# Kernel optimization log

Hardware: AMD Instinct MI355X
Metric: run time of the kernel (lower is better)

## Reference

```python
import jax, jax.numpy as jnp
import numpy as np

EPS = 0.0  # init eps

def setup_inputs() -> dict:
    key = jax.random.key(0)
    k1, k2, k3 = jax.random.split(key, 3)
    n_nodes = 100000
    n_edges = 6400000
    edge_weight = jax.random.uniform(k1, (n_edges,), dtype=jnp.float32)  # non-negative, required by norm='both'
    src = jax.random.randint(k2, (n_edges,), 0, n_nodes, dtype=jnp.int32)
    dst = jax.random.randint(k3, (n_edges,), 0, n_nodes, dtype=jnp.int32)
    return {"edge_weight": edge_weight, "src": src, "dst": dst, "num_nodes": n_nodes}

def reference(edge_weight, src, dst, num_nodes):
    # norm='both': out-degree (weighted) per source node via reversed graph,
    # in-degree (weighted) per destination node; both as segment sums over edges.
    out_deg = jax.ops.segment_sum(edge_weight, src, num_segments=num_nodes) + EPS
    in_deg = jax.ops.segment_sum(edge_weight, dst, num_segments=num_nodes) + EPS
    src_norm = out_deg ** -0.5  # [N]
    dst_norm = in_deg ** -0.5   # [N]
    # gather per-edge norms and multiply with edge weight
    return src_norm[src] * dst_norm[dst] * edge_weight
```

## Files before the change

kernel.cpp:

```cpp
#include <hip/hip_runtime.h>
#include <hip/hip_fp16.h>


#define N_NODES 100000
#define TWO_N   (2 * N_NODES)
#define THREADS 1024
#define GBLK    1024
#define KMAX    7
#define SCALE_F   512.0f
#define INV_SCALE 0.001953125f

__global__ __launch_bounds__(THREADS)
void hist_kernel(const float4* __restrict__ w4,
                 const int4* __restrict__ src4,
                 const int4* __restrict__ dst4,
                 const float* __restrict__ w,
                 const int* __restrict__ src,
                 const int* __restrict__ dst,
                 unsigned* __restrict__ parts,
                 int n4, int n_edges, int P, int C, int bins, int chunk4,
                 int swz)
{
    extern __shared__ unsigned lds[];
    int j, c;
    if (swz) {
        const int x = blockIdx.x & 7;
        const int r = blockIdx.x >> 3;
        j = r % P;
        c = x + 8 * (r / P);
    } else {
        j = blockIdx.x / C;
        c = blockIdx.x - j * C;
    }
    const int lo = j * bins;

    for (int k = threadIdx.x; k < bins; k += THREADS) lds[k] = 0;
    __syncthreads();

    const int beg = c * chunk4;
    const int end = min(n4, beg + chunk4);

#define QUAD(wv, sv, dv)                                                      \
    do {                                                                      \
        unsigned v0 = (unsigned)((wv).x * SCALE_F + 0.5f);                    \
        unsigned v1 = (unsigned)((wv).y * SCALE_F + 0.5f);                    \
        unsigned v2 = (unsigned)((wv).z * SCALE_F + 0.5f);                    \
        unsigned v3 = (unsigned)((wv).w * SCALE_F + 0.5f);                    \
        int a0 = (sv).x - lo, a1 = (sv).y - lo, a2 = (sv).z - lo, a3 = (sv).w - lo; \
        int b0 = (dv).x - lo, b1 = (dv).y - lo, b2 = (dv).z - lo, b3 = (dv).w - lo; \
        if ((unsigned)a0 < (unsigned)bins) atomicAdd(&lds[a0], v0);           \
        if ((unsigned)a1 < (unsigned)bins) atomicAdd(&lds[a1], v1);           \
        if ((unsigned)a2 < (unsigned)bins) atomicAdd(&lds[a2], v2);           \
        if ((unsigned)a3 < (unsigned)bins) atomicAdd(&lds[a3], v3);           \
        if ((unsigned)b0 < (unsigned)bins) atomicAdd(&lds[b0], v0 << 16);     \
        if ((unsigned)b1 < (unsigned)bins) atomicAdd(&lds[b1], v1 << 16);     \
        if ((unsigned)b2 < (unsigned)bins) atomicAdd(&lds[b2], v2 << 16);     \
        if ((unsigned)b3 < (unsigned)bins) atomicAdd(&lds[b3], v3 << 16);     \
    } while (0)

    int i = beg + (int)threadIdx.x;
    for (; i + 3 * THREADS < end; i += 4 * THREADS) {
        float4 wa = w4[i];
        float4 wb = w4[i + THREADS];
        float4 wc = w4[i + 2 * THREADS];
        float4 wd = w4[i + 3 * THREADS];
        int4 sa = src4[i];
        int4 sb = src4[i + THREADS];
        int4 sc = src4[i + 2 * THREADS];
        int4 sd = src4[i + 3 * THREADS];
        int4 da = dst4[i];
        int4 db = dst4[i + THREADS];
        int4 dc = dst4[i + 2 * THREADS];
        int4 dd = dst4[i + 3 * THREADS];
        QUAD(wa, sa, da);
        QUAD(wb, sb, db);
        QUAD(wc, sc, dc);
        QUAD(wd, sd, dd);
    }
    for (; i < end; i += THREADS) {
        float4 wa = w4[i];
        int4 sa = src4[i];
        int4 da = dst4[i];
        QUAD(wa, sa, da);
    }
#undef QUAD

    if (c == C - 1 && threadIdx.x == 0) {
        for (int e = n4 * 4; e < n_edges; ++e) {
            unsigned v = (unsigned)(w[e] * SCALE_F + 0.5f);
            int a = src[e] - lo;
            int b = dst[e] - lo;
            if ((unsigned)a < (unsigned)bins) atomicAdd(&lds[a], v);
            if ((unsigned)b < (unsigned)bins) atomicAdd(&lds[b], v << 16);
        }
    }

    __syncthreads();
    unsigned* op = parts + ((size_t)j * C + c) * bins;
    for (int k = threadIdx.x; k < bins; k += THREADS)
        __builtin_nontemporal_store(lds[k], op + k);
}

__global__ void reduce_rsqrt_kernel(const unsigned* __restrict__ parts,
                                    __half* __restrict__ normh,
                                    int P, int C, int bins)
{
    int i = blockIdx.x * blockDim.x + threadIdx.x;
    if (i >= N_NODES) return;
    int p = i / bins;
    int b = i - p * bins;
    const unsigned* base = parts + ((size_t)p * C) * bins + b;
    unsigned lo0 = 0, hi0 = 0, lo1 = 0, hi1 = 0, lo2 = 0, hi2 = 0, lo3 = 0, hi3 = 0;
    int c = 0;
    for (; c + 3 < C; c += 4) {
        unsigned v0 = base[(size_t)(c + 0) * bins];
        unsigned v1 = base[(size_t)(c + 1) * bins];
        unsigned v2 = base[(size_t)(c + 2) * bins];
        unsigned v3 = base[(size_t)(c + 3) * bins];
        lo0 += v0 & 0xFFFFu; hi0 += v0 >> 16;
        lo1 += v1 & 0xFFFFu; hi1 += v1 >> 16;
        lo2 += v2 & 0xFFFFu; hi2 += v2 >> 16;
        lo3 += v3 & 0xFFFFu; hi3 += v3 >> 16;
    }
    for (; c < C; ++c) {
        unsigned v = base[(size_t)c * bins];
        lo0 += v & 0xFFFFu; hi0 += v >> 16;
    }
    unsigned lo_s = lo0 + lo1 + lo2 + lo3;
    unsigned hi_s = hi0 + hi1 + hi2 + hi3;
    normh[i]           = __float2half(1.0f / sqrtf((float)lo_s * INV_SCALE));
    normh[N_NODES + i] = __float2half(1.0f / sqrtf((float)hi_s * INV_SCALE));
}

__global__ void degree_atomic_kernel(const float* __restrict__ w,
                                     const int* __restrict__ src,
                                     const int* __restrict__ dst,
                                     float* __restrict__ deg,
                                     int n_edges)
{
    int i = blockIdx.x * blockDim.x + threadIdx.x;
    int stride = gridDim.x * blockDim.x;
    for (; i < n_edges; i += stride) {
        float wi = w[i];
        atomicAdd(&deg[src[i]], wi);
        atomicAdd(&deg[N_NODES + dst[i]], wi);
    }
}

__global__ void rsqrt_half_kernel(const float* __restrict__ deg,
                                  __half* __restrict__ normh, int n)
{
    int i = blockIdx.x * blockDim.x + threadIdx.x;
    if (i < n) normh[i] = __float2half(1.0f / sqrtf(deg[i]));
}

__global__ __launch_bounds__(GBLK)
void prod_kernel(const float4* __restrict__ w4,
                 const int4* __restrict__ src4,
                 const int4* __restrict__ dst4,
                 const __half* __restrict__ srcn_h,
                 const __half* __restrict__ dstn_h,
                 float4* __restrict__ out4,
                 int n4, int n_edges, int qpb, int binsh,
                 const float* __restrict__ w,
                 const int* __restrict__ src,
                 const int* __restrict__ dst,
                 float* __restrict__ out)
{
    extern __shared__ __half lh[];
    const int q0   = blockIdx.x * qpb;
    const int qend = min(n4, q0 + qpb);
    const int t    = threadIdx.x;

    float4 pr[KMAX];
    int4   sv[KMAX], dv[KMAX];
    bool   val[KMAX];

#pragma unroll
    for (int k = 0; k < KMAX; ++k) {
        const int q = q0 + k * GBLK + t;
        val[k] = q < qend;
        if (val[k]) {
            pr[k] = w4[q];
            sv[k] = src4[q];
            dv[k] = dst4[q];
        }
    }

    for (int phase = 0; phase < 2; ++phase) {
        const __half* tab = phase ? dstn_h : srcn_h;
        for (int lo = 0; lo < N_NODES; lo += binsh) {
            const int len = min(binsh, N_NODES - lo);
            const int len8 = len >> 3;
            const uint4* tsrc = (const uint4*)(tab + lo);
            uint4* ldst = (uint4*)lh;
            for (int k2 = t; k2 < len8; k2 += GBLK) ldst[k2] = tsrc[k2];
            for (int k2 = (len8 << 3) + t; k2 < len; k2 += GBLK) lh[k2] = tab[lo + k2];
            __syncthreads();

#pragma unroll
            for (int k = 0; k < KMAX; ++k) {
                if (!val[k]) continue;
                const int4 iv = phase ? dv[k] : sv[k];
                unsigned a;
                a = (unsigned)(iv.x - lo); if (a < (unsigned)len) pr[k].x *= __half2float(lh[a]);
                a = (unsigned)(iv.y - lo); if (a < (unsigned)len) pr[k].y *= __half2float(lh[a]);
                a = (unsigned)(iv.z - lo); if (a < (unsigned)len) pr[k].z *= __half2float(lh[a]);
                a = (unsigned)(iv.w - lo); if (a < (unsigned)len) pr[k].w *= __half2float(lh[a]);
            }
            __syncthreads();
        }
    }

#pragma unroll
    for (int k = 0; k < KMAX; ++k) {
        const int q = q0 + k * GBLK + t;
        if (val[k]) out4[q] = pr[k];
    }

    if (blockIdx.x == 0 && t == 0) {
        for (int e = n4 * 4; e < n_edges; ++e)
            out[e] = __half2float(srcn_h[src[e]]) * __half2float(dstn_h[dst[e]]) * w[e];
    }
}

extern "C" void kernel_launch(void* const* d_in, const int* in_sizes, int n_in,
                              void* d_out, int out_size, void* d_ws, size_t ws_size,
                              hipStream_t stream)
{
    const float* w   = (const float*)d_in[0];
    const int*   src = (const int*)d_in[1];
    const int*   dst = (const int*)d_in[2];
    const int E  = in_sizes[0];
    const int n4 = E >> 2;
    float* out = (float*)d_out;

    __half* normh = (__half*)d_ws;
    char* scratch = (char*)d_ws + (1 << 20);
    unsigned* parts = (unsigned*)scratch;
    float* degf = (float*)scratch;
    size_t avail_u = (ws_size > (1u << 20)) ? (ws_size - (1 << 20)) / 4 : 0;

    const int cands[3] = {163840, 131072, 81920};
    int lds_hist = 65536;
    for (int tC = 0; tC < 3; ++tC)
        if (hipFuncSetAttribute((const void*)hist_kernel,
                                hipFuncAttributeMaxDynamicSharedMemorySize,
                                cands[tC]) == hipSuccess) { lds_hist = cands[tC]; break; }
    int lds_prod = 65536;
    for (int tC = 0; tC < 3; ++tC)
        if (hipFuncSetAttribute((const void*)prod_kernel,
                                hipFuncAttributeMaxDynamicSharedMemorySize,
                                cands[tC]) == hipSuccess) { lds_prod = cands[tC]; break; }

    const int bins = lds_hist / 4;
    const int P = (N_NODES + bins - 1) / bins;

    const int blk_per_cu = 163840 / lds_hist;
    int C = (256 * blk_per_cu) / P;
    const size_t per_chunk_u = (size_t)P * (size_t)bins;
    if (avail_u < per_chunk_u) C = 0;
    else {
        int cmax = (int)(avail_u / per_chunk_u);
        if (C > cmax) C = cmax;
    }

    int swz = 0;
    if (C >= 8) { C &= ~7; swz = 1; }

    if (C >= 1) {
        const int chunk4 = (n4 + C - 1) / C;
        hist_kernel<<<P * C, THREADS, (size_t)lds_hist, stream>>>(
            (const float4*)w, (const int4*)src, (const int4*)dst,
            w, src, dst, parts, n4, E, P, C, bins, chunk4, swz);
        reduce_rsqrt_kernel<<<(N_NODES + 255) / 256, 256, 0, stream>>>(
            parts, normh, P, C, bins);
    } else {
        hipMemsetAsync(degf, 0, (size_t)TWO_N * sizeof(float), stream);
        degree_atomic_kernel<<<2048, 256, 0, stream>>>(w, src, dst, degf, E);
        rsqrt_half_kernel<<<(TWO_N + 255) / 256, 256, 0, stream>>>(degf, normh, TWO_N);
    }

    {
        const int binsh = lds_prod / 2;
        const int maxq = KMAX * GBLK;
        int C2 = (n4 + maxq - 1) / maxq;
        if (C2 < 256) C2 = 256;
        const int qpb = (n4 + C2 - 1) / C2;
        prod_kernel<<<C2, GBLK, (size_t)lds_prod, stream>>>(
            (const float4*)w, (const int4*)src, (const int4*)dst,
            normh, normh + N_NODES, (float4*)out,
            n4, E, qpb, binsh, w, src, dst, out);
    }
}
```

Before: 71.91 us.

## Software-pipeline histogram loads with double-buffered register prefetch

Replaces the 4-way unrolled load-then-atomic loop with a two-element-per-trip software pipeline. The next iteration's float4/int4 loads are issued before the current LDS atomics, and a sched_barrier stops the compiler from reordering them. It also adds a min-blocks hint of 4 to launch_bounds, which may limit registers. The aim is to hide global load latency behind LDS atomic work, at the cost of fewer loads in flight per trip than the old 4-way unroll.

```diff
diff --git a/kernel.cpp b/kernel.cpp
--- a/kernel.cpp
+++ b/kernel.cpp
@@ -10,7 +10,7 @@
 #define SCALE_F   512.0f
 #define INV_SCALE 0.001953125f
 
-__global__ __launch_bounds__(THREADS)
+__global__ __launch_bounds__(THREADS, 4)
 void hist_kernel(const float4* __restrict__ w4,
                  const int4* __restrict__ src4,
                  const int4* __restrict__ dst4,
@@ -39,6 +39,7 @@
 
     const int beg = c * chunk4;
     const int end = min(n4, beg + chunk4);
+    const int t   = threadIdx.x;
 
 #define QUAD(wv, sv, dv)                                                      \
     do {                                                                      \
@@ -58,30 +59,36 @@
         if ((unsigned)b3 < (unsigned)bins) atomicAdd(&lds[b3], v3 << 16);     \
     } while (0)
 
-    int i = beg + (int)threadIdx.x;
-    for (; i + 3 * THREADS < end; i += 4 * THREADS) {
-        float4 wa = w4[i];
-        float4 wb = w4[i + THREADS];
-        float4 wc = w4[i + 2 * THREADS];
-        float4 wd = w4[i + 3 * THREADS];
-        int4 sa = src4[i];
-        int4 sb = src4[i + THREADS];
-        int4 sc = src4[i + 2 * THREADS];
-        int4 sd = src4[i + 3 * THREADS];
-        int4 da = dst4[i];
-        int4 db = dst4[i + THREADS];
-        int4 dc = dst4[i + 2 * THREADS];
-        int4 dd = dst4[i + 3 * THREADS];
-        QUAD(wa, sa, da);
-        QUAD(wb, sb, db);
-        QUAD(wc, sc, dc);
-        QUAD(wd, sd, dd);
-    }
-    for (; i < end; i += THREADS) {
-        float4 wa = w4[i];
-        int4 sa = src4[i];
-        int4 da = dst4[i];
-        QUAD(wa, sa, da);
+    {
+        const int total = end - beg;
+        const int trips = (total + 2 * THREADS - 1) / (2 * THREADS);
+        int i = beg + t;
+
+        float4 wc0, wc1, wn0, wn1;
+        int4   sc0, sc1, sn0, sn1, dc0, dc1, dn0, dn1;
+        bool   pc0, pc1, pn0, pn1;
+
+        pn0 = i < end;
+        pn1 = (i + THREADS) < end;
+        if (pn0) { wn0 = w4[i];           sn0 = src4[i];           dn0 = dst4[i]; }
+        if (pn1) { wn1 = w4[i + THREADS]; sn1 = src4[i + THREADS]; dn1 = dst4[i + THREADS]; }
+
+        for (int tr = 0; tr < trips; ++tr) {
+            wc0 = wn0; sc0 = sn0; dc0 = dn0; pc0 = pn0;
+            wc1 = wn1; sc1 = sn1; dc1 = dn1; pc1 = pn1;
+
+            const int ni = i + 2 * THREADS;
+            pn0 = (tr + 1 < trips) && (ni < end);
+            pn1 = (tr + 1 < trips) && ((ni + THREADS) < end);
+            if (pn0) { wn0 = w4[ni];           sn0 = src4[ni];           dn0 = dst4[ni]; }
+            if (pn1) { wn1 = w4[ni + THREADS]; sn1 = src4[ni + THREADS]; dn1 = dst4[ni + THREADS]; }
+
+            __builtin_amdgcn_sched_barrier(0);
+
+            if (pc0) QUAD(wc0, sc0, dc0);
+            if (pc1) QUAD(wc1, sc1, dc1);
+            i = ni;
+        }
     }
 #undef QUAD
 
```

Measured after the change: 72.26 us. No clear change (+0.5%).
